# Kernel tuning notes

Measured on AMD Instinct MI355X. Metric: run time of the kernel, lower is better.

The kernel has to match this reference:

```python
import jax, jax.numpy as jnp
import numpy as np

N_NODES = 100000
N_EDGES = 1600000
IN_DIM, HID_DIM, OUT_DIM = 256, 128, 128


def gcn_norm(edge_index, edge_weight, num_nodes):
    # Add self-loops with weight 1 (PyG GCNConv default fill_value=1.0)
    loop = jnp.arange(num_nodes, dtype=edge_index.dtype)
    src = jnp.concatenate([edge_index[0], loop])
    dst = jnp.concatenate([edge_index[1], loop])
    w = jnp.concatenate([edge_weight, jnp.ones((num_nodes,), edge_weight.dtype)])
    # Symmetric normalization: deg computed at destination over edge weights
    deg = jax.ops.segment_sum(w, dst, num_segments=num_nodes)
    dinv = jnp.where(deg > 0, jax.lax.rsqrt(deg), 0.0)
    norm = dinv[src] * w * dinv[dst]  # [E + N]
    return src, dst, norm


def gcn_conv(x, W, b, src, dst, norm, num_nodes):
    h = x @ W                                  # [N, out]
    msg = h[src] * norm[:, None]               # gather + scale, [E+N, out]
    out = jax.ops.segment_sum(msg, dst, num_segments=num_nodes)  # scatter-add
    return out + b


def setup_inputs() -> dict:
    key = jax.random.key(0)
    ks = jax.random.split(key, 8)
    x = jax.random.normal(ks[0], (N_NODES, IN_DIM), dtype=jnp.float32)
    edge_index = jax.random.randint(ks[1], (2, N_EDGES), 0, N_NODES, dtype=jnp.int64)
    edge_weight = jax.random.uniform(ks[2], (N_EDGES,), dtype=jnp.float32)
    s1 = 1.0 / np.sqrt(IN_DIM)
    s2 = 1.0 / np.sqrt(HID_DIM)
    W1 = jax.random.uniform(ks[3], (IN_DIM, HID_DIM), jnp.float32, -s1, s1)
    b1 = jnp.zeros((HID_DIM,), jnp.float32)
    W2 = jax.random.uniform(ks[4], (HID_DIM, OUT_DIM), jnp.float32, -s2, s2)
    b2 = jnp.zeros((OUT_DIM,), jnp.float32)
    return {"x": x, "edge_index": edge_index, "edge_weight": edge_weight,
            "W1": W1, "b1": b1, "W2": W2, "b2": b2}


def reference(x, edge_index, edge_weight, W1, b1, W2, b2):
    n = x.shape[0]
    src, dst, norm = gcn_norm(edge_index, edge_weight, n)
    h = jax.nn.relu(gcn_conv(x, W1, b1, src, dst, norm, n))
    out = gcn_conv(h, W2, b2, src, dst, norm, n)
    return out
```

## Files before the change

kernel.cpp:

```cpp
#include <hip/hip_runtime.h>
#include <stdint.h>

#define N_NODES 100000
#define N_EDGES 1600000
#define IN_DIM 256
#define HID_DIM 128
#define OUT_DIM 128

#define NBUCK 391
#define CHUNK 2048

typedef __attribute__((ext_vector_type(8))) short short8;
typedef __attribute__((ext_vector_type(4))) float floatx4;

__device__ __forceinline__ float bf2f(unsigned short u) {
    union { unsigned int i; float f; } v; v.i = ((unsigned int)u) << 16; return v.f;
}
__device__ __forceinline__ unsigned short f2bf(float f) {
    union { float fl; unsigned int i; } v; v.fl = f;
    unsigned int x = v.i;
    return (unsigned short)((x + 0x7fffu + ((x >> 16) & 1u)) >> 16);
}
__device__ __forceinline__ float bflo(unsigned int u) {
    union { unsigned int i; float f; } v; v.i = u << 16; return v.f;
}
__device__ __forceinline__ float bfhi(unsigned int u) {
    union { unsigned int i; float f; } v; v.i = u & 0xffff0000u; return v.f;
}
__device__ __forceinline__ float asf(unsigned int u) {
    union { unsigned int i; float f; } v; v.i = u; return v.f;
}
__device__ __forceinline__ unsigned int asu(float f) {
    union { float fl; unsigned int i; } v; v.fl = f; return v.i;
}
__device__ __forceinline__ unsigned int pack2(float a, float b) {
    unsigned int ua = asu(a), ub = asu(b);
    ua += 0x7fffu + ((ua >> 16) & 1u);
    ub += 0x7fffu + ((ub >> 16) & 1u);
    return (ua >> 16) | (ub & 0xffff0000u);
}
__device__ __forceinline__ short8 pack8(float4 a, float4 b) {
    union { unsigned int u[4]; short8 s; } r;
    r.u[0] = pack2(a.x, a.y);
    r.u[1] = pack2(a.z, a.w);
    r.u[2] = pack2(b.x, b.y);
    r.u[3] = pack2(b.z, b.w);
    return r.s;
}

__global__ void k_detect(const unsigned int* __restrict__ xu, const unsigned int* __restrict__ eu,
                         int* __restrict__ flags, int* __restrict__ bucket_cnt) {
    __shared__ int s_huge, s_odd;
    if (threadIdx.x == 0) { s_huge = 0; s_odd = 0; }
    if (threadIdx.x < NBUCK) bucket_cnt[threadIdx.x] = 0;
    __syncthreads();
    int huge = 0, odd = 0;
    for (int i = threadIdx.x; i < 1024; i += 512) {
        unsigned int b = xu[i];
        unsigned int e = (b >> 23) & 0xffu;
        if (e >= 0xf0u) huge = 1;
        if (eu[2 * i + 1] != 0) odd = 1;
    }
    if (huge) atomicOr(&s_huge, 1);
    if (odd) atomicOr(&s_odd, 1);
    __syncthreads();
    if (threadIdx.x == 0) { flags[0] = s_huge ? 0 : 1; flags[1] = s_odd ? 0 : 1; }
}

__device__ __forceinline__ int load_idx(const void* base, long long i, int i64m) {
    int v = i64m ? (int)((const long long*)base)[i] : ((const int*)base)[i];
    return v < 0 ? 0 : (v >= N_NODES ? N_NODES - 1 : v);
}
__device__ __forceinline__ float load_f(const void* base, long long i, int f32m) {
    return f32m ? ((const float*)base)[i] : bf2f(((const unsigned short*)base)[i]);
}

__global__ void k_bhist(const void* __restrict__ ei, const int* __restrict__ flags,
                        int* __restrict__ bucket_cnt, int e) {
    __shared__ int h[NBUCK];
    for (int t = threadIdx.x; t < NBUCK; t += 256) h[t] = 0;
    __syncthreads();
    int i64m = flags[1];
    int base = blockIdx.x * CHUNK;
    int end = base + CHUNK < e ? base + CHUNK : e;
    for (int i = base + threadIdx.x; i < end; i += 256) {
        int d = load_idx(ei, (long long)N_EDGES + i, i64m);
        atomicAdd(&h[d >> 8], 1);
    }
    __syncthreads();
    for (int t = threadIdx.x; t < NBUCK; t += 256)
        if (h[t]) atomicAdd(&bucket_cnt[t], h[t]);
}

__global__ void k_bscan(const int* __restrict__ bucket_cnt, int* __restrict__ bucket_base,
                        int* __restrict__ bucket_cursor, int* __restrict__ rowptr) {
    __shared__ int lds[512];
    int t = threadIdx.x;
    int v = (t < NBUCK) ? bucket_cnt[t] : 0;
    lds[t] = v;
    __syncthreads();
    for (int off = 1; off < 512; off <<= 1) {
        int x = (t >= off) ? lds[t - off] : 0;
        __syncthreads();
        lds[t] += x;
        __syncthreads();
    }
    int excl = lds[t] - v;
    if (t < NBUCK) { bucket_base[t] = excl; bucket_cursor[t] = excl; }
    if (t == 0) { bucket_base[NBUCK] = lds[NBUCK - 1]; rowptr[N_NODES] = N_EDGES; }
}

__global__ void k_bscatter(const void* __restrict__ ei, const void* __restrict__ ew,
                           const int* __restrict__ flags, int* __restrict__ bucket_cursor,
                           uint2* __restrict__ ebuf, int e) {
    __shared__ int h[NBUCK];
    for (int t = threadIdx.x; t < NBUCK; t += 256) h[t] = 0;
    __syncthreads();
    int f32m = flags[0], i64m = flags[1];
    int base = blockIdx.x * CHUNK;
    int end = base + CHUNK < e ? base + CHUNK : e;
    for (int i = base + threadIdx.x; i < end; i += 256) {
        int d = load_idx(ei, (long long)N_EDGES + i, i64m);
        atomicAdd(&h[d >> 8], 1);
    }
    __syncthreads();
    for (int t = threadIdx.x; t < NBUCK; t += 256) {
        int c = h[t];
        h[t] = c ? atomicAdd(&bucket_cursor[t], c) : 0;
    }
    __syncthreads();
    for (int i = base + threadIdx.x; i < end; i += 256) {
        int s = load_idx(ei, i, i64m);
        int d = load_idx(ei, (long long)N_EDGES + i, i64m);
        float w = load_f(ew, i, f32m);
        int b = d >> 8;
        int p = atomicAdd(&h[b], 1);
        uint2 c; c.x = (unsigned int)s | ((unsigned int)(d & 255) << 17); c.y = asu(w);
        ebuf[p] = c;
    }
}

__global__ void k_fine(const uint2* __restrict__ ebuf, const int* __restrict__ bucket_base,
                       uint2* __restrict__ csr, int* __restrict__ rowptr,
                       float* __restrict__ dinv, int n) {
    __shared__ int h[256];
    __shared__ float fw[256];
    __shared__ int c2[256];
    int t = threadIdx.x, b = blockIdx.x;
    int e0 = bucket_base[b], e1 = bucket_base[b + 1];
    if (t < 256) { h[t] = 0; fw[t] = 0.f; }
    __syncthreads();
    for (int i = e0 + t; i < e1; i += 512) {
        uint2 c = ebuf[i];
        int dl = (c.x >> 17) & 255;
        atomicAdd(&h[dl], 1);
        atomicAdd(&fw[dl], asf(c.y));
    }
    __syncthreads();
    int own = (t < 256) ? h[t] : 0;
    for (int off = 1; off < 256; off <<= 1) {
        int x = (t >= off && t < 256) ? h[t - off] : 0;
        __syncthreads();
        if (t < 256) h[t] += x;
        __syncthreads();
    }
    if (t < 256) {
        int excl = h[t] - own;
        int node = (b << 8) + t;
        if (node < n) {
            rowptr[node] = e0 + excl;
            dinv[node] = rsqrtf(1.0f + fw[t]);
        }
        c2[t] = e0 + excl;
    }
    __syncthreads();
    for (int i = e0 + t; i < e1; i += 512) {
        uint2 c = ebuf[i];
        int dl = (c.x >> 17) & 255;
        int p = atomicAdd(&c2[dl], 1);
        csr[p] = c;
    }
}

__global__ void k_fold(uint4* __restrict__ csr4, const float* __restrict__ dinv, int npair) {
    int i = blockIdx.x * 256 + threadIdx.x;
    if (i >= npair) return;
    uint4 c = csr4[i];
    c.y = asu(asf(c.y) * dinv[c.x & 0x1FFFF]);
    c.w = asu(asf(c.w) * dinv[c.z & 0x1FFFF]);
    csr4[i] = c;
}

__global__ void k_transpose(const void* __restrict__ W1, const void* __restrict__ W2,
                            const int* __restrict__ flags,
                            unsigned short* __restrict__ W1T, unsigned short* __restrict__ W2T) {
    int i = blockIdx.x * 256 + threadIdx.x;
    int f32m = flags[0];
    if (i < IN_DIM * HID_DIM) {
        int k = i / HID_DIM, n = i % HID_DIM;
        W1T[n * IN_DIM + k] = f2bf(load_f(W1, i, f32m));
    } else {
        int j = i - IN_DIM * HID_DIM;
        if (j < HID_DIM * OUT_DIM) {
            int k = j / OUT_DIM, n = j % OUT_DIM;
            W2T[n * HID_DIM + k] = f2bf(load_f(W2, j, f32m));
        }
    }
}

template <int KH, bool F32M>
__device__ __forceinline__ void gemm_loop(const void* __restrict__ A,
                                          const unsigned short* __restrict__ Bs,
                                          size_t aoff, int quad, int l16, floatx4 (&acc)[8]) {
    constexpr int NCH = KH / 32;
    constexpr int BMASK = KH / 8 - 1;
    short8 a[NCH];
    if (F32M) {
        const float* ap = (const float*)A;
#pragma unroll
        for (int ch = 0; ch < NCH; ch++) {
            float4 f0 = *(const float4*)(ap + aoff + ch * 32);
            float4 f1 = *(const float4*)(ap + aoff + ch * 32 + 4);
            a[ch] = pack8(f0, f1);
        }
    } else {
        const unsigned short* ap = (const unsigned short*)A;
#pragma unroll
        for (int ch = 0; ch < NCH; ch++)
            a[ch] = *(const short8*)(ap + aoff + ch * 32);
    }
#pragma unroll
    for (int ch = 0; ch < NCH; ch++) {
#pragma unroll
        for (int c = 0; c < 8; c++) {
            int col = c * 16 + l16;
            int boff = col * KH + 8 * ((ch * 4 + quad + (col & 7)) & BMASK);
            short8 bf = *(const short8*)(Bs + boff);
            acc[c] = __builtin_amdgcn_mfma_f32_16x16x32_bf16(a[ch], bf, acc[c], 0, 0, 0);
        }
    }
}

template <int K, bool RAWA>
__global__ void k_gemm(const void* __restrict__ A, const unsigned short* __restrict__ WT,
                       unsigned short* __restrict__ H, const int* __restrict__ flags, int n) {
    constexpr int KH = (K > 128) ? 128 : K;
    __shared__ unsigned short Bs[128 * KH];

    int wave = threadIdx.x >> 6;
    int lane = threadIdx.x & 63;
    int quad = lane >> 4;
    int l16 = lane & 15;
    int rowbase = blockIdx.x * 64 + wave * 16;
    int r0 = rowbase + l16;        if (r0 >= n) r0 = n - 1;
    size_t aoff0 = (size_t)r0 * K + quad * 8;

    floatx4 acc[8];
#pragma unroll
    for (int c = 0; c < 8; c++) acc[c] = (floatx4){0.f, 0.f, 0.f, 0.f};

    int f32m = RAWA ? flags[0] : 0;

#pragma unroll
    for (int hh = 0; hh < K / KH; hh++) {
        if (hh) __syncthreads();
        for (int base = threadIdx.x * 8; base < 128 * KH; base += 256 * 8) {
            int col = base / KH;
            int k = base - col * KH;
            int ks = (k + (col & 7) * 8) & (KH - 1);
            *(short8*)(&Bs[col * KH + ks]) = *(const short8*)(WT + col * K + hh * KH + k);
        }
        __syncthreads();
        if (RAWA && f32m)
            gemm_loop<KH, true>(A, Bs, aoff0 + hh * KH, quad, l16, acc);
        else
            gemm_loop<KH, false>(A, Bs, aoff0 + hh * KH, quad, l16, acc);
    }

#pragma unroll
    for (int c = 0; c < 8; c++)
#pragma unroll
        for (int r = 0; r < 4; r++) {
            int grow = rowbase + quad * 4 + r;
            if (grow < n) H[(size_t)grow * 128 + c * 16 + l16] = f2bf(acc[c][r]);
        }
}

#define NODES_PER_BLK 32

__device__ __forceinline__ void acc8(float wt, uint4 hv, float* a) {
    a[0] += wt * bflo(hv.x); a[1] += wt * bfhi(hv.x);
    a[2] += wt * bflo(hv.y); a[3] += wt * bfhi(hv.y);
    a[4] += wt * bflo(hv.z); a[5] += wt * bfhi(hv.z);
    a[6] += wt * bflo(hv.w); a[7] += wt * bfhi(hv.w);
}

template <bool RELU, bool FINAL>
__global__ void k_aggregate(const unsigned short* __restrict__ H, const int* __restrict__ rowptr,
                            const uint2* __restrict__ csr, const float* __restrict__ dinv,
                            const void* __restrict__ bias, void* __restrict__ out,
                            const int* __restrict__ flags, int n) {
    __shared__ int cursor;
    if (threadIdx.x == 0) cursor = 0;
    __syncthreads();
    int lane = threadIdx.x & 15;
    int col = lane * 8;
    int f32m = flags[0];

    float bv[8];
#pragma unroll
    for (int i = 0; i < 8; i++) bv[i] = load_f(bias, col + i, f32m);

    for (;;) {
        int idx;
        if (lane == 0) idx = atomicAdd(&cursor, 1);
        idx = __shfl(idx, 0, 16);
        if (idx >= NODES_PER_BLK) break;
        int node = blockIdx.x * NODES_PER_BLK + idx;
        if (node >= n) break;

        int e0 = rowptr[node], e1 = rowptr[node + 1];
        uint4 u = *(const uint4*)(H + (size_t)node * 128 + col);
        float dn = dinv[node];

        float a[8] = {0.f, 0.f, 0.f, 0.f, 0.f, 0.f, 0.f, 0.f};
        int e = e0;
        for (; e + 4 <= e1; e += 4) {
            uint2 c0 = csr[e], c1 = csr[e + 1], c2 = csr[e + 2], c3 = csr[e + 3];
            uint4 h0 = *(const uint4*)(H + (size_t)(c0.x & 0x1FFFF) * 128 + col);
            uint4 h1 = *(const uint4*)(H + (size_t)(c1.x & 0x1FFFF) * 128 + col);
            uint4 h2 = *(const uint4*)(H + (size_t)(c2.x & 0x1FFFF) * 128 + col);
            uint4 h3 = *(const uint4*)(H + (size_t)(c3.x & 0x1FFFF) * 128 + col);
            acc8(asf(c0.y), h0, a); acc8(asf(c1.y), h1, a);
            acc8(asf(c2.y), h2, a); acc8(asf(c3.y), h3, a);
        }
        for (; e < e1; e++) {
            uint2 c = csr[e];
            uint4 hh = *(const uint4*)(H + (size_t)(c.x & 0x1FFFF) * 128 + col);
            acc8(asf(c.y), hh, a);
        }

        float coef = dn * dn;
        a[0] = dn * a[0] + coef * bflo(u.x) + bv[0];
        a[1] = dn * a[1] + coef * bfhi(u.x) + bv[1];
        a[2] = dn * a[2] + coef * bflo(u.y) + bv[2];
        a[3] = dn * a[3] + coef * bfhi(u.y) + bv[3];
        a[4] = dn * a[4] + coef * bflo(u.z) + bv[4];
        a[5] = dn * a[5] + coef * bfhi(u.z) + bv[5];
        a[6] = dn * a[6] + coef * bflo(u.w) + bv[6];
        a[7] = dn * a[7] + coef * bfhi(u.w) + bv[7];

        if (RELU) {
#pragma unroll
            for (int i = 0; i < 8; i++) a[i] = fmaxf(a[i], 0.f);
        }
        if (FINAL && f32m) {
            float* op = (float*)out + (size_t)node * 128 + col;
            float4 o0 = {a[0], a[1], a[2], a[3]};
            float4 o1 = {a[4], a[5], a[6], a[7]};
            *(float4*)op = o0;
            *(float4*)(op + 4) = o1;
        } else {
            uint4 o;
            o.x = pack2(a[0], a[1]); o.y = pack2(a[2], a[3]);
            o.z = pack2(a[4], a[5]); o.w = pack2(a[6], a[7]);
            *(uint4*)((unsigned short*)out + (size_t)node * 128 + col) = o;
        }
    }
}

extern "C" void kernel_launch(void* const* d_in, const int* in_sizes, int n_in,
                              void* d_out, int out_size, void* d_ws, size_t ws_size,
                              hipStream_t stream) {
    const void* x  = d_in[0];
    const void* ei = d_in[1];
    const void* ew = d_in[2];
    const void* W1 = d_in[3];
    const void* b1 = d_in[4];
    const void* W2 = d_in[5];
    const void* b2 = d_in[6];

    char* p = (char*)d_ws;
    auto alloc = [&](size_t bytes) { char* r = p; p += (bytes + 255) & ~(size_t)255; return r; };
    int*   flags    = (int*)alloc(256);
    float* dinv     = (float*)alloc((size_t)N_NODES * 4);
    int*   rowptr   = (int*)alloc((size_t)(N_NODES + 1) * 4);
    int*   bucket_cnt    = (int*)alloc((size_t)NBUCK * 4);
    int*   bucket_base   = (int*)alloc((size_t)(NBUCK + 1) * 4);
    int*   bucket_cursor = (int*)alloc((size_t)NBUCK * 4);
    uint2* csr      = (uint2*)alloc((size_t)N_EDGES * 8);
    unsigned short* W1T  = (unsigned short*)alloc((size_t)IN_DIM * HID_DIM * 2);
    unsigned short* W2T  = (unsigned short*)alloc((size_t)HID_DIM * OUT_DIM * 2);
    unsigned short* hbuf = (unsigned short*)alloc((size_t)N_NODES * 128 * 2);
    unsigned short* zbuf = (unsigned short*)alloc((size_t)N_NODES * 128 * 2);
    uint2* ebuf = (uint2*)hbuf;

    int nbC = (N_EDGES + CHUNK - 1) / CHUNK;
    int nbG = (N_NODES + 63) / 64;
    int nbA = (N_NODES + NODES_PER_BLK - 1) / NODES_PER_BLK;
    int nbF = (N_EDGES / 2 + 255) / 256;

    k_detect<<<1, 512, 0, stream>>>((const unsigned int*)x, (const unsigned int*)ei, flags, bucket_cnt);
    k_bhist<<<nbC, 256, 0, stream>>>(ei, flags, bucket_cnt, N_EDGES);
    k_bscan<<<1, 512, 0, stream>>>(bucket_cnt, bucket_base, bucket_cursor, rowptr);
    k_bscatter<<<nbC, 256, 0, stream>>>(ei, ew, flags, bucket_cursor, ebuf, N_EDGES);
    k_fine<<<NBUCK, 512, 0, stream>>>(ebuf, bucket_base, csr, rowptr, dinv, N_NODES);
    k_fold<<<nbF, 256, 0, stream>>>((uint4*)csr, dinv, N_EDGES / 2);
    k_transpose<<<(IN_DIM * HID_DIM + HID_DIM * OUT_DIM + 255) / 256, 256, 0, stream>>>(W1, W2, flags, W1T, W2T);

    k_gemm<IN_DIM, true><<<nbG, 256, 0, stream>>>(x, W1T, hbuf, flags, N_NODES);
    k_aggregate<true, false><<<nbA, 256, 0, stream>>>(hbuf, rowptr, csr, dinv,
                                                      b1, zbuf, flags, N_NODES);
    k_gemm<HID_DIM, false><<<nbG, 256, 0, stream>>>(zbuf, W2T, hbuf, flags, N_NODES);
    k_aggregate<false, true><<<nbA, 256, 0, stream>>>(hbuf, rowptr, csr, dinv,
                                                      b2, d_out, flags, N_NODES);
}
```

Baseline: 447.7 us.

## Fold source dinv into GEMM epilogue, reuse block histograms, drop fold kernel

The source-side normalization dinv[src] is moved out of the per-edge CSR weights and applied per row in the GEMM epilogue, so the separate k_fold pass over the CSR is removed. The aggregate epilogue is reworked to match, and the self-loop term now uses the prescaled h. k_bhist saves its per-block histograms so k_bscatter no longer recomputes them with a second read of the destination indices. The GEMM K-half tile drops to 64, the aggregate uses 16 nodes per block, and the epilogue stores are reordered per row; the extra per-block histogram buffer costs some workspace.

```diff
diff --git a/kernel.cpp b/kernel.cpp
--- a/kernel.cpp
+++ b/kernel.cpp
@@ -76,7 +76,7 @@
 }
 
 __global__ void k_bhist(const void* __restrict__ ei, const int* __restrict__ flags,
-                        int* __restrict__ bucket_cnt, int e) {
+                        int* __restrict__ bucket_cnt, int* __restrict__ blockhist, int e) {
     __shared__ int h[NBUCK];
     for (int t = threadIdx.x; t < NBUCK; t += 256) h[t] = 0;
     __syncthreads();
@@ -88,8 +88,12 @@
         atomicAdd(&h[d >> 8], 1);
     }
     __syncthreads();
-    for (int t = threadIdx.x; t < NBUCK; t += 256)
-        if (h[t]) atomicAdd(&bucket_cnt[t], h[t]);
+    int* bh = blockhist + (size_t)blockIdx.x * NBUCK;
+    for (int t = threadIdx.x; t < NBUCK; t += 256) {
+        int v = h[t];
+        bh[t] = v;
+        if (v) atomicAdd(&bucket_cnt[t], v);
+    }
 }
 
 __global__ void k_bscan(const int* __restrict__ bucket_cnt, int* __restrict__ bucket_base,
@@ -112,23 +116,17 @@
 
 __global__ void k_bscatter(const void* __restrict__ ei, const void* __restrict__ ew,
                            const int* __restrict__ flags, int* __restrict__ bucket_cursor,
-                           uint2* __restrict__ ebuf, int e) {
+                           uint2* __restrict__ ebuf, const int* __restrict__ blockhist, int e) {
     __shared__ int h[NBUCK];
-    for (int t = threadIdx.x; t < NBUCK; t += 256) h[t] = 0;
+    const int* bh = blockhist + (size_t)blockIdx.x * NBUCK;
+    for (int t = threadIdx.x; t < NBUCK; t += 256) {
+        int c = bh[t];
+        h[t] = c ? atomicAdd(&bucket_cursor[t], c) : 0;
+    }
     __syncthreads();
     int f32m = flags[0], i64m = flags[1];
     int base = blockIdx.x * CHUNK;
     int end = base + CHUNK < e ? base + CHUNK : e;
-    for (int i = base + threadIdx.x; i < end; i += 256) {
-        int d = load_idx(ei, (long long)N_EDGES + i, i64m);
-        atomicAdd(&h[d >> 8], 1);
-    }
-    __syncthreads();
-    for (int t = threadIdx.x; t < NBUCK; t += 256) {
-        int c = h[t];
-        h[t] = c ? atomicAdd(&bucket_cursor[t], c) : 0;
-    }
-    __syncthreads();
     for (int i = base + threadIdx.x; i < end; i += 256) {
         int s = load_idx(ei, i, i64m);
         int d = load_idx(ei, (long long)N_EDGES + i, i64m);
@@ -180,15 +178,6 @@
         int p = atomicAdd(&c2[dl], 1);
         csr[p] = c;
     }
-}
-
-__global__ void k_fold(uint4* __restrict__ csr4, const float* __restrict__ dinv, int npair) {
-    int i = blockIdx.x * 256 + threadIdx.x;
-    if (i >= npair) return;
-    uint4 c = csr4[i];
-    c.y = asu(asf(c.y) * dinv[c.x & 0x1FFFF]);
-    c.w = asu(asf(c.w) * dinv[c.z & 0x1FFFF]);
-    csr4[i] = c;
 }
 
 __global__ void k_transpose(const void* __restrict__ W1, const void* __restrict__ W2,
@@ -243,8 +232,9 @@
 
 template <int K, bool RAWA>
 __global__ void k_gemm(const void* __restrict__ A, const unsigned short* __restrict__ WT,
-                       unsigned short* __restrict__ H, const int* __restrict__ flags, int n) {
-    constexpr int KH = (K > 128) ? 128 : K;
+                       const float* __restrict__ dinv, unsigned short* __restrict__ H,
+                       const int* __restrict__ flags, int n) {
+    constexpr int KH = 64;
     __shared__ unsigned short Bs[128 * KH];
 
     int wave = threadIdx.x >> 6;
@@ -278,15 +268,18 @@
     }
 
 #pragma unroll
-    for (int c = 0; c < 8; c++)
-#pragma unroll
-        for (int r = 0; r < 4; r++) {
-            int grow = rowbase + quad * 4 + r;
-            if (grow < n) H[(size_t)grow * 128 + c * 16 + l16] = f2bf(acc[c][r]);
-        }
-}
-
-#define NODES_PER_BLK 32
+    for (int r = 0; r < 4; r++) {
+        int grow = rowbase + quad * 4 + r;
+        if (grow < n) {
+            float sc = dinv[grow];
+#pragma unroll
+            for (int c = 0; c < 8; c++)
+                H[(size_t)grow * 128 + c * 16 + l16] = f2bf(sc * acc[c][r]);
+        }
+    }
+}
+
+#define NODES_PER_BLK 16
 
 __device__ __forceinline__ void acc8(float wt, uint4 hv, float* a) {
     a[0] += wt * bflo(hv.x); a[1] += wt * bfhi(hv.x);
@@ -340,15 +333,14 @@
             acc8(asf(c.y), hh, a);
         }
 
-        float coef = dn * dn;
-        a[0] = dn * a[0] + coef * bflo(u.x) + bv[0];
-        a[1] = dn * a[1] + coef * bfhi(u.x) + bv[1];
-        a[2] = dn * a[2] + coef * bflo(u.y) + bv[2];
-        a[3] = dn * a[3] + coef * bfhi(u.y) + bv[3];
-        a[4] = dn * a[4] + coef * bflo(u.z) + bv[4];
-        a[5] = dn * a[5] + coef * bfhi(u.z) + bv[5];
-        a[6] = dn * a[6] + coef * bflo(u.w) + bv[6];
-        a[7] = dn * a[7] + coef * bfhi(u.w) + bv[7];
+        a[0] = dn * (a[0] + bflo(u.x)) + bv[0];
+        a[1] = dn * (a[1] + bfhi(u.x)) + bv[1];
+        a[2] = dn * (a[2] + bflo(u.y)) + bv[2];
+        a[3] = dn * (a[3] + bfhi(u.y)) + bv[3];
+        a[4] = dn * (a[4] + bflo(u.z)) + bv[4];
+        a[5] = dn * (a[5] + bfhi(u.z)) + bv[5];
+        a[6] = dn * (a[6] + bflo(u.w)) + bv[6];
+        a[7] = dn * (a[7] + bfhi(u.w)) + bv[7];
 
         if (RELU) {
 #pragma unroll
@@ -393,25 +385,24 @@
     unsigned short* W2T  = (unsigned short*)alloc((size_t)HID_DIM * OUT_DIM * 2);
     unsigned short* hbuf = (unsigned short*)alloc((size_t)N_NODES * 128 * 2);
     unsigned short* zbuf = (unsigned short*)alloc((size_t)N_NODES * 128 * 2);
+    int nbC = (N_EDGES + CHUNK - 1) / CHUNK;
+    int*   blockhist = (int*)alloc((size_t)nbC * NBUCK * 4);
     uint2* ebuf = (uint2*)hbuf;
 
-    int nbC = (N_EDGES + CHUNK - 1) / CHUNK;
     int nbG = (N_NODES + 63) / 64;
     int nbA = (N_NODES + NODES_PER_BLK - 1) / NODES_PER_BLK;
-    int nbF = (N_EDGES / 2 + 255) / 256;
 
     k_detect<<<1, 512, 0, stream>>>((const unsigned int*)x, (const unsigned int*)ei, flags, bucket_cnt);
-    k_bhist<<<nbC, 256, 0, stream>>>(ei, flags, bucket_cnt, N_EDGES);
+    k_bhist<<<nbC, 256, 0, stream>>>(ei, flags, bucket_cnt, blockhist, N_EDGES);
     k_bscan<<<1, 512, 0, stream>>>(bucket_cnt, bucket_base, bucket_cursor, rowptr);
-    k_bscatter<<<nbC, 256, 0, stream>>>(ei, ew, flags, bucket_cursor, ebuf, N_EDGES);
+    k_bscatter<<<nbC, 256, 0, stream>>>(ei, ew, flags, bucket_cursor, ebuf, blockhist, N_EDGES);
     k_fine<<<NBUCK, 512, 0, stream>>>(ebuf, bucket_base, csr, rowptr, dinv, N_NODES);
-    k_fold<<<nbF, 256, 0, stream>>>((uint4*)csr, dinv, N_EDGES / 2);
     k_transpose<<<(IN_DIM * HID_DIM + HID_DIM * OUT_DIM + 255) / 256, 256, 0, stream>>>(W1, W2, flags, W1T, W2T);
 
-    k_gemm<IN_DIM, true><<<nbG, 256, 0, stream>>>(x, W1T, hbuf, flags, N_NODES);
+    k_gemm<IN_DIM, true><<<nbG, 256, 0, stream>>>(x, W1T, dinv, hbuf, flags, N_NODES);
     k_aggregate<true, false><<<nbA, 256, 0, stream>>>(hbuf, rowptr, csr, dinv,
                                                       b1, zbuf, flags, N_NODES);
-    k_gemm<HID_DIM, false><<<nbG, 256, 0, stream>>>(zbuf, W2T, hbuf, flags, N_NODES);
+    k_gemm<HID_DIM, false><<<nbG, 256, 0, stream>>>(zbuf, W2T, dinv, hbuf, flags, N_NODES);
     k_aggregate<false, true><<<nbA, 256, 0, stream>>>(hbuf, rowptr, csr, dinv,
                                                       b2, d_out, flags, N_NODES);
 }
```

New measurement: 442.1 us. About the same (-1.3%).
